# Kernel optimization log

Measured on AMD Instinct MI355X. Metric: run time of the kernel, lower is better.

Reference implementation:

```python
import jax, jax.numpy as jnp
import numpy as np

B, S, R, L, Z = 2048, 277, 80, 12, 56


def setup_inputs() -> dict:
    key = jax.random.key(0)
    k0, k1, k2, k3, k4, k5 = jax.random.split(key, 6)
    true_idx = jax.random.randint(k0, (B, S), 0, R)
    x = jax.nn.one_hot(true_idx, R, dtype=jnp.float32)            # one-hot true rules
    recon_x = jax.nn.softmax(jax.random.normal(k1, (B, S, R)), axis=-1)  # post-softmax probs
    mu = jax.random.normal(k2, (B, Z), dtype=jnp.float32)
    log_var = jax.random.normal(k3, (B, Z), dtype=jnp.float32)
    ind_to_lhs_ind = jax.random.randint(k4, (R,), 0, L)
    masks = (jax.random.uniform(k5, (L, R)) > 0.5).astype(jnp.float32)
    # a valid grammar always allows the true rule under its own LHS mask
    masks = masks.at[ind_to_lhs_ind, jnp.arange(R)].set(1.0)
    return {"x": x, "recon_x": recon_x, "mu": mu, "log_var": log_var,
            "masks": masks, "ind_to_lhs_ind": ind_to_lhs_ind}


def reference(x, recon_x, mu, log_var, masks, ind_to_lhs_ind):
    batch_size, seq_len, n_rules = x.shape
    z_size = mu.shape[1]
    # apply_masks: fused gather + mask + renormalize (replaces B*S python loop)
    true_rule = jnp.argmax(x, axis=-1)                 # [B,S]
    mask = masks[ind_to_lhs_ind[true_rule]]            # [B,S,R]
    x_resc = recon_x * mask
    out = x_resc / jnp.sum(x_resc, axis=-1, keepdims=True)
    # BCELoss(size_average=False): torch clamps log terms at -100
    log_p = jnp.clip(jnp.log(out), -100.0, None)
    log_1mp = jnp.clip(jnp.log1p(-out), -100.0, None)
    bce = -jnp.sum(x * log_p + (1.0 - x) * log_1mp) / (seq_len * batch_size)
    # sample_z == False branch: moment-matching error
    avg_mu = jnp.sum(mu, axis=0) / batch_size          # [Z]
    var = jnp.matmul(mu.T, mu) / batch_size            # [Z,Z]
    var_err = var - jnp.eye(z_size, dtype=mu.dtype)
    mom_err = jnp.sum(avg_mu * avg_mu) / z_size + jnp.sum(jnp.abs(var_err)) / (z_size * z_size)
    return bce + mom_err
```

## Files before the change

kernel.cpp:

```cpp
#include <hip/hip_runtime.h>
#include <math.h>

#define Bn 2048
#define Sn 277
#define Rn 80
#define Ln 12
#define Zn 56
#define NROWS (Bn * Sn)
#define ROWS_PER_BLK 64
#define NBLK_BCE (NROWS / ROWS_PER_BLK)
#define NMOM 8
#define NBLK_TOT (NBLK_BCE + NMOM)
#define NWAVE_BCE (NBLK_BCE * 4)

#define WS_CM  0
#define WS_BCE 1280
#define WS_VAR 143104
#define WS_AVG 155648

__device__ __forceinline__ float qsum4(float v) {
    int t = __builtin_amdgcn_update_dpp(0, __float_as_int(v), 0xB1, 0xF, 0xF, true);
    v += __int_as_float(t);
    t = __builtin_amdgcn_update_dpp(0, __float_as_int(v), 0x4E, 0xF, 0xF, true);
    v += __int_as_float(t);
    return v;
}

__global__ __launch_bounds__(256) void setup_kernel(
    const float* __restrict__ masks, const int* __restrict__ lhs, char* __restrict__ ws)
{
    unsigned* cmask_sw = (unsigned*)(ws + WS_CM);
    for (int idx = threadIdx.x; idx < Rn * 4; idx += 256) {
        const int r = idx >> 2, c = idx & 3;
        const int l = lhs[r];
        unsigned bits = 0u;
        for (int k = 0; k < 5; ++k)
            for (int comp = 0; comp < 4; ++comp) {
                const int j = 16 * k + 4 * c + comp;
                if (masks[l * Rn + j] > 0.5f) bits |= (1u << (4 * k + comp));
            }
        cmask_sw[idx] = bits;
    }
}

__global__ __launch_bounds__(256) void main_kernel(
    const float* __restrict__ x, const float* __restrict__ recon,
    const float* __restrict__ mu, char* __restrict__ ws)
{
    const int tid = threadIdx.x;

    if (blockIdx.x < NMOM) {
        float* var_g = (float*)(ws + WS_VAR);
        float* avg_g = (float*)(ws + WS_AVG);
        __shared__ float sm[32 * Zn];

        const int m = blockIdx.x;
        float acc[13];
        #pragma unroll
        for (int k = 0; k < 13; ++k) acc[k] = 0.0f;
        float asum = 0.0f;

        for (int ch = 0; ch < 8; ++ch) {
            __syncthreads();
            const float* src = mu + ((size_t)m * 256 + ch * 32) * Zn;
            #pragma unroll
            for (int i = 0; i < 7; ++i) sm[tid + 256 * i] = src[tid + 256 * i];
            __syncthreads();

            #pragma unroll
            for (int k = 0; k < 13; ++k) {
                const int p = tid + 256 * k;
                if (p < Zn * Zn) {
                    const int i = p / Zn, j = p - i * Zn;
                    float a = 0.0f;
                    #pragma unroll 8
                    for (int r = 0; r < 32; ++r) a = fmaf(sm[r * Zn + i], sm[r * Zn + j], a);
                    acc[k] += a;
                }
            }
            if (tid < Zn) {
                float s = 0.0f;
                #pragma unroll 8
                for (int r = 0; r < 32; ++r) s += sm[r * Zn + tid];
                asum += s;
            }
        }
        #pragma unroll
        for (int k = 0; k < 13; ++k) {
            const int p = tid + 256 * k;
            if (p < Zn * Zn) atomicAdd(&var_g[p], acc[k]);
        }
        if (tid < Zn) atomicAdd(&avg_g[tid], asum);
        return;
    }

    const int bid = blockIdx.x - NMOM;
    const unsigned* cmask_sw = (const unsigned*)(ws + WS_CM);
    float* bce_partial = (float*)(ws + WS_BCE);

    const int lrow = tid >> 2;
    const int c = tid & 3;
    const size_t row = (size_t)bid * ROWS_PER_BLK + lrow;
    const float4* xp = (const float4*)(x + row * Rn);
    const float4* rp = (const float4*)(recon + row * Rn);

    const float4 xv0 = xp[c];
    const float4 xv1 = xp[c + 4];
    const float4 xv2 = xp[c + 8];
    const float4 xv3 = xp[c + 12];
    const float4 xv4 = xp[c + 16];
    const float4 rv0 = rp[c];
    const float4 rv1 = rp[c + 4];
    const float4 rv2 = rp[c + 8];
    const float4 rv3 = rp[c + 12];
    const float4 rv4 = rp[c + 16];

    auto dotc = [](const float4 v, float base) {
        return fmaf(v.x, base, fmaf(v.y, base + 1.f, fmaf(v.z, base + 2.f, v.w * (base + 3.f))));
    };
    float dl = dotc(xv0, 0.f) + dotc(xv1, 16.f) + dotc(xv2, 32.f)
             + dotc(xv3, 48.f) + dotc(xv4, 64.f);
    const float xs = ((xv0.x + xv0.y) + (xv0.z + xv0.w)) + ((xv1.x + xv1.y) + (xv1.z + xv1.w))
                   + ((xv2.x + xv2.y) + (xv2.z + xv2.w)) + ((xv3.x + xv3.y) + (xv3.z + xv3.w))
                   + ((xv4.x + xv4.y) + (xv4.z + xv4.w));
    dl = fmaf((float)(4 * c), xs, dl);
    const int amax = (int)(qsum4(dl) + 0.5f);

    const unsigned bits = cmask_sw[(amax << 2) | c];

    auto mskd = [&](float4 v, int k) -> float4 {
        float4 r;
        r.x = ((bits >> (4 * k + 0)) & 1u) ? v.x : 0.f;
        r.y = ((bits >> (4 * k + 1)) & 1u) ? v.y : 0.f;
        r.z = ((bits >> (4 * k + 2)) & 1u) ? v.z : 0.f;
        r.w = ((bits >> (4 * k + 3)) & 1u) ? v.w : 0.f;
        return r;
    };
    const float4 m0 = mskd(rv0, 0);
    const float4 m1 = mskd(rv1, 1);
    const float4 m2 = mskd(rv2, 2);
    const float4 m3 = mskd(rv3, 3);
    const float4 m4 = mskd(rv4, 4);

    float dd = ((m0.x + m0.y) + (m0.z + m0.w)) + ((m1.x + m1.y) + (m1.z + m1.w))
             + ((m2.x + m2.y) + (m2.z + m2.w)) + ((m3.x + m3.y) + (m3.z + m3.w))
             + ((m4.x + m4.y) + (m4.z + m4.w));
    const float invd = __builtin_amdgcn_rcpf(qsum4(dd));

    const int ka = amax >> 4;
    const int ca = (amax >> 2) & 3;
    const int comp = amax & 3;
    const bool owner = (c == ca);

    float ss = 0.0f;
    float ta = 1.0f;
    auto acc = [&](const float4 m, int k) {
        const float t0 = fminf(m.x * invd, 1.f);
        const float t1 = fminf(m.y * invd, 1.f);
        const float t2 = fminf(m.z * invd, 1.f);
        const float t3 = fminf(m.w * invd, 1.f);
        ss += fmaxf(__logf(1.f - t0), -100.f) + fmaxf(__logf(1.f - t1), -100.f)
            + fmaxf(__logf(1.f - t2), -100.f) + fmaxf(__logf(1.f - t3), -100.f);
        if (owner && k == ka)
            ta = (comp == 0) ? t0 : (comp == 1) ? t1 : (comp == 2) ? t2 : t3;
    };
    acc(m0, 0); acc(m1, 1); acc(m2, 2); acc(m3, 3); acc(m4, 4);
    if (owner)
        ss += fmaxf(__logf(ta), -100.f) - fmaxf(__logf(1.f - ta), -100.f);

    ss = qsum4(ss);
    ss += __shfl_xor(ss, 4);
    ss += __shfl_xor(ss, 8);
    ss += __shfl_xor(ss, 16);
    ss += __shfl_xor(ss, 32);
    if ((tid & 63) == 0)
        bce_partial[bid * 4 + (tid >> 6)] = ss;
}

__global__ __launch_bounds__(256) void finalize_kernel(
    const char* __restrict__ ws, float* __restrict__ out)
{
    const float* bce_partial = (const float*)(ws + WS_BCE);
    const float* var_g = (const float*)(ws + WS_VAR);
    const float* avg_g = (const float*)(ws + WS_AVG);
    __shared__ double sb[4];
    __shared__ float sv[4], sa[4];
    const int tid = threadIdx.x;

    double bsum = 0.0;
    for (int i = tid; i < NWAVE_BCE; i += 256) bsum += (double)bce_partial[i];

    float vsum = 0.0f;
    for (int p = tid; p < Zn * Zn; p += 256) {
        const int i = p / Zn, j = p - i * Zn;
        const float e = var_g[p] * (1.0f / (float)Bn) - ((i == j) ? 1.0f : 0.0f);
        vsum += fabsf(e);
    }
    float asum = 0.0f;
    for (int z = tid; z < Zn; z += 256) { const float a = avg_g[z]; asum += a * a; }

    #pragma unroll
    for (int o = 32; o; o >>= 1) {
        bsum += __shfl_xor(bsum, o);
        vsum += __shfl_xor(vsum, o);
        asum += __shfl_xor(asum, o);
    }
    if ((tid & 63) == 0) { const int w = tid >> 6; sb[w] = bsum; sv[w] = vsum; sa[w] = asum; }
    __syncthreads();
    if (tid == 0) {
        const double tb = (sb[0] + sb[1]) + (sb[2] + sb[3]);
        const double tv = (double)((sv[0] + sv[1]) + (sv[2] + sv[3]));
        const double ta = (double)((sa[0] + sa[1]) + (sa[2] + sa[3]));
        const double bce = -tb / ((double)Sn * (double)Bn);
        const double mom = ta / ((double)Bn * (double)Bn * (double)Zn)
                         + tv / ((double)Zn * (double)Zn);
        out[0] = (float)(bce + mom);
    }
}

extern "C" void kernel_launch(void* const* d_in, const int* in_sizes, int n_in,
                              void* d_out, int out_size, void* d_ws, size_t ws_size,
                              hipStream_t stream)
{
    const float* x     = (const float*)d_in[0];
    const float* recon = (const float*)d_in[1];
    const float* mu    = (const float*)d_in[2];
    const float* masks = (const float*)d_in[4];
    const int*   lhs   = (const int*)d_in[5];
    float* out = (float*)d_out;
    char* ws = (char*)d_ws;

    hipMemsetAsync(ws + WS_VAR, 0, 12544 + 224, stream);
    setup_kernel<<<1, 256, 0, stream>>>(masks, lhs, ws);
    main_kernel<<<NBLK_TOT, 256, 0, stream>>>(x, recon, mu, ws);
    finalize_kernel<<<1, 256, 0, stream>>>(ws, out);
}
```

Baseline: 405.2 us.

## Process four rows per quad and replace per-element logs with a single product log

Each thread group of four lanes now handles four consecutive rows, loading all 40 float4s up front behind a scheduling barrier so more memory requests are in flight per thread. The sum of log(1-t) terms becomes the log of a running product, falling back to the clamped per-element path when the product underflows to zero. This cuts transcendental work and block count, at the cost of higher register pressure (launch_bounds 256,2) and small numerical differences from accumulating a product instead of a sum.

New measurement: 381.3 us. 1.06x faster.

```diff
diff --git a/kernel.cpp b/kernel.cpp
--- a/kernel.cpp
+++ b/kernel.cpp
@@ -7,7 +7,7 @@
 #define Ln 12
 #define Zn 56
 #define NROWS (Bn * Sn)
-#define ROWS_PER_BLK 64
+#define ROWS_PER_BLK 256
 #define NBLK_BCE (NROWS / ROWS_PER_BLK)
 #define NMOM 8
 #define NBLK_TOT (NBLK_BCE + NMOM)
@@ -15,8 +15,8 @@
 
 #define WS_CM  0
 #define WS_BCE 1280
-#define WS_VAR 143104
-#define WS_AVG 155648
+#define WS_VAR 36736
+#define WS_AVG 49280
 
 __device__ __forceinline__ float qsum4(float v) {
     int t = __builtin_amdgcn_update_dpp(0, __float_as_int(v), 0xB1, 0xF, 0xF, true);
@@ -43,7 +43,7 @@
     }
 }
 
-__global__ __launch_bounds__(256) void main_kernel(
+__global__ __launch_bounds__(256, 2) void main_kernel(
     const float* __restrict__ x, const float* __restrict__ recon,
     const float* __restrict__ mu, char* __restrict__ ws)
 {
@@ -98,75 +98,94 @@
     const unsigned* cmask_sw = (const unsigned*)(ws + WS_CM);
     float* bce_partial = (float*)(ws + WS_BCE);
 
-    const int lrow = tid >> 2;
+    const int q = tid >> 2;
     const int c = tid & 3;
-    const size_t row = (size_t)bid * ROWS_PER_BLK + lrow;
-    const float4* xp = (const float4*)(x + row * Rn);
-    const float4* rp = (const float4*)(recon + row * Rn);
-
-    const float4 xv0 = xp[c];
-    const float4 xv1 = xp[c + 4];
-    const float4 xv2 = xp[c + 8];
-    const float4 xv3 = xp[c + 12];
-    const float4 xv4 = xp[c + 16];
-    const float4 rv0 = rp[c];
-    const float4 rv1 = rp[c + 4];
-    const float4 rv2 = rp[c + 8];
-    const float4 rv3 = rp[c + 12];
-    const float4 rv4 = rp[c + 16];
+    const size_t row0 = (size_t)bid * ROWS_PER_BLK + 4 * (size_t)q;
+    const float4* xp0 = (const float4*)(x + row0 * Rn);
+    const float4* rp0 = (const float4*)(recon + row0 * Rn);
+
+    float4 X[4][5], Rv[4][5];
+    #pragma unroll
+    for (int j = 0; j < 4; ++j)
+        #pragma unroll
+        for (int k = 0; k < 5; ++k)
+            X[j][k] = xp0[20 * j + c + 4 * k];
+    #pragma unroll
+    for (int j = 0; j < 4; ++j)
+        #pragma unroll
+        for (int k = 0; k < 5; ++k)
+            Rv[j][k] = rp0[20 * j + c + 4 * k];
+    __builtin_amdgcn_sched_barrier(0);
 
     auto dotc = [](const float4 v, float base) {
         return fmaf(v.x, base, fmaf(v.y, base + 1.f, fmaf(v.z, base + 2.f, v.w * (base + 3.f))));
     };
-    float dl = dotc(xv0, 0.f) + dotc(xv1, 16.f) + dotc(xv2, 32.f)
-             + dotc(xv3, 48.f) + dotc(xv4, 64.f);
-    const float xs = ((xv0.x + xv0.y) + (xv0.z + xv0.w)) + ((xv1.x + xv1.y) + (xv1.z + xv1.w))
-                   + ((xv2.x + xv2.y) + (xv2.z + xv2.w)) + ((xv3.x + xv3.y) + (xv3.z + xv3.w))
-                   + ((xv4.x + xv4.y) + (xv4.z + xv4.w));
-    dl = fmaf((float)(4 * c), xs, dl);
-    const int amax = (int)(qsum4(dl) + 0.5f);
-
-    const unsigned bits = cmask_sw[(amax << 2) | c];
-
-    auto mskd = [&](float4 v, int k) -> float4 {
-        float4 r;
-        r.x = ((bits >> (4 * k + 0)) & 1u) ? v.x : 0.f;
-        r.y = ((bits >> (4 * k + 1)) & 1u) ? v.y : 0.f;
-        r.z = ((bits >> (4 * k + 2)) & 1u) ? v.z : 0.f;
-        r.w = ((bits >> (4 * k + 3)) & 1u) ? v.w : 0.f;
-        return r;
-    };
-    const float4 m0 = mskd(rv0, 0);
-    const float4 m1 = mskd(rv1, 1);
-    const float4 m2 = mskd(rv2, 2);
-    const float4 m3 = mskd(rv3, 3);
-    const float4 m4 = mskd(rv4, 4);
-
-    float dd = ((m0.x + m0.y) + (m0.z + m0.w)) + ((m1.x + m1.y) + (m1.z + m1.w))
-             + ((m2.x + m2.y) + (m2.z + m2.w)) + ((m3.x + m3.y) + (m3.z + m3.w))
-             + ((m4.x + m4.y) + (m4.z + m4.w));
-    const float invd = __builtin_amdgcn_rcpf(qsum4(dd));
-
-    const int ka = amax >> 4;
-    const int ca = (amax >> 2) & 3;
-    const int comp = amax & 3;
-    const bool owner = (c == ca);
 
     float ss = 0.0f;
-    float ta = 1.0f;
-    auto acc = [&](const float4 m, int k) {
-        const float t0 = fminf(m.x * invd, 1.f);
-        const float t1 = fminf(m.y * invd, 1.f);
-        const float t2 = fminf(m.z * invd, 1.f);
-        const float t3 = fminf(m.w * invd, 1.f);
-        ss += fmaxf(__logf(1.f - t0), -100.f) + fmaxf(__logf(1.f - t1), -100.f)
-            + fmaxf(__logf(1.f - t2), -100.f) + fmaxf(__logf(1.f - t3), -100.f);
-        if (owner && k == ka)
-            ta = (comp == 0) ? t0 : (comp == 1) ? t1 : (comp == 2) ? t2 : t3;
-    };
-    acc(m0, 0); acc(m1, 1); acc(m2, 2); acc(m3, 3); acc(m4, 4);
-    if (owner)
-        ss += fmaxf(__logf(ta), -100.f) - fmaxf(__logf(1.f - ta), -100.f);
+    #pragma unroll
+    for (int j = 0; j < 4; ++j) {
+        float dl = dotc(X[j][0], 0.f) + dotc(X[j][1], 16.f) + dotc(X[j][2], 32.f)
+                 + dotc(X[j][3], 48.f) + dotc(X[j][4], 64.f);
+        float xs = 0.f;
+        #pragma unroll
+        for (int k = 0; k < 5; ++k)
+            xs += ((X[j][k].x + X[j][k].y) + (X[j][k].z + X[j][k].w));
+        dl = fmaf((float)(4 * c), xs, dl);
+        const int amax = (int)(qsum4(dl) + 0.5f);
+
+        const unsigned bits = cmask_sw[(amax << 2) | c];
+
+        float4 M[5];
+        #pragma unroll
+        for (int k = 0; k < 5; ++k) {
+            M[k].x = ((bits >> (4 * k + 0)) & 1u) ? Rv[j][k].x : 0.f;
+            M[k].y = ((bits >> (4 * k + 1)) & 1u) ? Rv[j][k].y : 0.f;
+            M[k].z = ((bits >> (4 * k + 2)) & 1u) ? Rv[j][k].z : 0.f;
+            M[k].w = ((bits >> (4 * k + 3)) & 1u) ? Rv[j][k].w : 0.f;
+        }
+        float dd = 0.f;
+        #pragma unroll
+        for (int k = 0; k < 5; ++k)
+            dd += ((M[k].x + M[k].y) + (M[k].z + M[k].w));
+        const float invd = __builtin_amdgcn_rcpf(qsum4(dd));
+
+        const int ka = amax >> 4;
+        const int ca = (amax >> 2) & 3;
+        const int comp = amax & 3;
+        const bool owner = (c == ca);
+
+        float p = 1.0f;
+        float ta = 1.0f;
+        #pragma unroll
+        for (int k = 0; k < 5; ++k) {
+            const float t0 = fminf(M[k].x * invd, 1.f);
+            const float t1 = fminf(M[k].y * invd, 1.f);
+            const float t2 = fminf(M[k].z * invd, 1.f);
+            const float t3 = fminf(M[k].w * invd, 1.f);
+            p *= ((1.f - t0) * (1.f - t1)) * ((1.f - t2) * (1.f - t3));
+            if (owner && k == ka)
+                ta = (comp == 0) ? t0 : (comp == 1) ? t1 : (comp == 2) ? t2 : t3;
+        }
+        if (p > 0.0f) {
+            ss += __builtin_amdgcn_logf(p) * 0.69314718055994531f;
+        } else {
+            const float4* rpj = rp0 + 20 * j;
+            #pragma unroll
+            for (int k = 0; k < 5; ++k) {
+                const float4 v = rpj[c + 4 * k];
+                const float w0 = ((bits >> (4 * k + 0)) & 1u) ? v.x : 0.f;
+                const float w1 = ((bits >> (4 * k + 1)) & 1u) ? v.y : 0.f;
+                const float w2 = ((bits >> (4 * k + 2)) & 1u) ? v.z : 0.f;
+                const float w3 = ((bits >> (4 * k + 3)) & 1u) ? v.w : 0.f;
+                ss += fmaxf(__logf(1.f - fminf(w0 * invd, 1.f)), -100.f)
+                    + fmaxf(__logf(1.f - fminf(w1 * invd, 1.f)), -100.f)
+                    + fmaxf(__logf(1.f - fminf(w2 * invd, 1.f)), -100.f)
+                    + fmaxf(__logf(1.f - fminf(w3 * invd, 1.f)), -100.f);
+            }
+        }
+        if (owner)
+            ss += fmaxf(__logf(ta), -100.f) - fmaxf(__logf(1.f - ta), -100.f);
+    }
 
     ss = qsum4(ss);
     ss += __shfl_xor(ss, 4);
```
